# Performance work log

Hardware: AMD Instinct MI355X
Metric: run time of the kernel (lower is better)

The kernel has to match this reference:

```python
import jax, jax.numpy as jnp
import numpy as np

# Irreps structure: (multiplicity, component dim 2l+1) for 64x0e + 32x1o + 16x2e
MULTS = (64, 32, 16)
DIMS = (1, 3, 5)
N_NODES = 65536
NUM_TYPES = 64


def setup_inputs() -> dict:
    key = jax.random.key(0)
    k_x, k_idx, k0, k1, k2 = jax.random.split(key, 5)
    dim = sum(m * d for m, d in zip(MULTS, DIMS))  # 240
    x = jax.random.normal(k_x, (N_NODES, dim), dtype=jnp.float32)
    idx = jax.random.randint(k_idx, (N_NODES,), 0, NUM_TYPES)
    W0 = jax.random.normal(k0, (NUM_TYPES, 64, 64), dtype=jnp.float32)
    W1 = jax.random.normal(k1, (NUM_TYPES, 32, 32), dtype=jnp.float32)
    W2 = jax.random.normal(k2, (NUM_TYPES, 16, 16), dtype=jnp.float32)
    return {"x": x, "W0": W0, "W1": W1, "W2": W2, "idx": idx}


def reference(x, W0, W1, W2, idx):
    """Indexed e3nn-style linear: per-node index gathers a weight set; each
    irrep block mixes multiplicity channels (shared across the 2l+1 components)
    with e3nn path normalization 1/sqrt(m_in)."""
    n = x.shape[0]
    outs = []
    off = 0
    for W, m, d in zip((W0, W1, W2), MULTS, DIMS):
        blk = x[:, off:off + m * d].reshape(n, m, d)  # [N, m_in, 2l+1]
        off += m * d
        Wn = W[idx]  # gather per-node weights: [N, m_in, m_out]
        scale = np.float32(1.0 / np.sqrt(m))
        out = jnp.einsum('nio,nid->nod', Wn, blk) * scale  # [N, m_out, 2l+1]
        outs.append(out.reshape(n, m * d))
    return jnp.concatenate(outs, axis=-1)
```

## Files before the change

kernel.cpp:

```cpp
#include <hip/hip_runtime.h>

typedef __attribute__((ext_vector_type(8))) short short8;
typedef __attribute__((ext_vector_type(4))) float floatx4;
typedef __attribute__((ext_vector_type(4))) unsigned uintx4;

#define NTYPES    64
#define WT_STRIDE 5632
#define WROWS     16
#define CPAD      16
#define RSTRIDE   976

__device__ __forceinline__ unsigned short f2bf(float f) {
    union { float f; unsigned u; } v; v.f = f;
    unsigned u = v.u;
    u += 0x7FFFu + ((u >> 16) & 1u);
    return (unsigned short)(u >> 16);
}

__device__ __forceinline__ unsigned pk2(float lo, float hi) {
    unsigned r;
    asm("v_cvt_pk_bf16_f32 %0, %1, %2" : "=v"(r) : "v"(lo), "v"(hi));
    return r;
}

__global__ __launch_bounds__(256) void wt_kernel(const float* __restrict__ W0,
                                                 const float* __restrict__ W1,
                                                 const float* __restrict__ W2,
                                                 const int* __restrict__ idx,
                                                 unsigned short* __restrict__ wt,
                                                 int* __restrict__ bh, int n) {
    __shared__ float ws0[4096];
    __shared__ float ws1[1024];
    __shared__ float ws2[256];
    __shared__ int hc[NTYPES];
    const int t = blockIdx.x, tid = threadIdx.x;
    if (tid < NTYPES) hc[tid] = 0;
    const float4* s0 = (const float4*)(W0 + (size_t)t * 4096);
#pragma unroll
    for (int j = 0; j < 4; ++j) ((float4*)ws0)[j * 256 + tid] = s0[j * 256 + tid];
    ((float4*)ws1)[tid] = ((const float4*)(W1 + (size_t)t * 1024))[tid];
    if (tid < 64) ((float4*)ws2)[tid] = ((const float4*)(W2 + (size_t)t * 256))[tid];
    __syncthreads();
    const int per = (n + NTYPES - 1) / NTYPES;
    for (int e = tid; e < per; e += 256) {
        int g = t * per + e;
        if (g < n) atomicAdd(&hc[idx[g]], 1);
    }
    unsigned short* dst = wt + (size_t)t * WT_STRIDE;
    for (int e = tid; e < 4096; e += 256) {
        int f = e >> 9, rem = e & 511, rr = rem >> 5, k2 = rem & 31;
        int i = (f & 1) * 32 + k2, o = (f >> 1) * 16 + rr;
        dst[e] = f2bf(ws0[i * 64 + o] * 0.125f);
    }
    for (int e = tid; e < 1024; e += 256) {
        int h = e >> 9, rem = e & 511, rr = rem >> 5, k = rem & 31;
        dst[4096 + e] = f2bf(ws1[k * 32 + h * 16 + rr] * 0.17677669529663687f);
    }
    for (int e = tid; e < 512; e += 256) {
        int rr = e >> 5, k = e & 31;
        dst[5120 + e] = (k < 16) ? f2bf(ws2[k * 16 + rr] * 0.25f) : (unsigned short)0;
    }
    __syncthreads();
    if (tid < NTYPES) bh[t * NTYPES + tid] = hc[tid];
}

__global__ __launch_bounds__(64) void base_kernel(const int* __restrict__ bh,
                                                  int* __restrict__ gcur) {
    const int t = threadIdx.x;
    int v = 0;
#pragma unroll
    for (int b = 0; b < NTYPES; ++b) v += bh[b * NTYPES + t];
    int s = v;
#pragma unroll
    for (int o = 1; o < 64; o <<= 1) {
        int u = __shfl_up(s, o);
        if (t >= o) s += u;
    }
    gcur[t * CPAD] = s - v;
}

__global__ __launch_bounds__(256) void scatter_kernel(const int* __restrict__ idx,
                                                      int* __restrict__ gcur,
                                                      int* __restrict__ psort, int n) {
    __shared__ int c[NTYPES], off[NTYPES], cur[NTYPES];
    const int tid = threadIdx.x, g = blockIdx.x * 256 + tid;
    if (tid < NTYPES) { c[tid] = 0; cur[tid] = 0; }
    __syncthreads();
    int ty = -1;
    if (g < n) { ty = idx[g]; atomicAdd(&c[ty], 1); }
    __syncthreads();
    if (tid < NTYPES && c[tid]) off[tid] = atomicAdd(&gcur[tid * CPAD], c[tid]);
    __syncthreads();
    if (g < n) {
        int rk = atomicAdd(&cur[ty], 1);
        psort[off[ty] + rk] = g | (ty << 24);
    }
}

#define LOAD_FRAGS(WB) do {                                         \
    const unsigned short* _wp = (WB) + r * 32 + q4 * 8;             \
    wa0 = *(const short8*)(_wp);                                    \
    wa1 = *(const short8*)(_wp + 512);                              \
    wa2 = *(const short8*)(_wp + 1024);                             \
    wa3 = *(const short8*)(_wp + 1536);                             \
    wa4 = *(const short8*)(_wp + 2048);                             \
    wa5 = *(const short8*)(_wp + 2560);                             \
    wa6 = *(const short8*)(_wp + 3072);                             \
    wa7 = *(const short8*)(_wp + 3584);                             \
    wc0 = *(const short8*)(_wp + 4096);                             \
    wc1 = *(const short8*)(_wp + 4608);                             \
    wc2 = *(const short8*)(_wp + 5120);                             \
} while (0)

__global__ __launch_bounds__(64) void main_kernel(
    const float* __restrict__ x,
    const int* __restrict__ psort,
    const unsigned short* __restrict__ wt,
    float* __restrict__ out, int n)
{
    __shared__ __align__(16) unsigned char xl[16384];
    const int ln = threadIdx.x;
    const int nbase = blockIdx.x * WROWS;
    if (nbase >= n) return;
    const int nv = min(WROWS, n - nbase);

    int pl = 0;
    if (ln < WROWS && (nbase + ln) < n) pl = psort[nbase + ln];

    const int r = ln & 15, q4 = ln >> 4;

    int ti  = __shfl(pl, r) >> 24;
    int tim = __shfl(pl, (r > 0) ? (r - 1) : 0) >> 24;
    bool bnd = (r == 0) || (ti != tim);
    unsigned m = (unsigned)(__ballot(bnd) & 0xFFFFull);
    const int ty0 = __shfl(pl, 0) >> 24;

#pragma unroll
    for (int k = 0; k < 16; ++k) {
        int L = k * 1024 + ln * 16;
        int row = (int)(((unsigned)(L >> 4) * 1075u) >> 16);
        int col = L - row * RSTRIDE;
        int node = __shfl(pl, min(row, 15)) & 0xFFFFFF;
        int colc = min(col, 944);
        const float* src = x + (size_t)node * 240 + (colc >> 2);
        __builtin_amdgcn_global_load_lds(
            (const __attribute__((address_space(1))) void*)src,
            (__attribute__((address_space(3))) void*)(xl + k * 1024),
            16, 0, 0);
    }

    short8 wa0, wa1, wa2, wa3, wa4, wa5, wa6, wa7, wc0, wc1, wc2;
    LOAD_FRAGS(wt + (size_t)ty0 * WT_STRIDE);

    asm volatile("s_waitcnt vmcnt(0)" ::: "memory");
    __builtin_amdgcn_sched_barrier(0);

    const float4* xr = (const float4*)(xl + r * RSTRIDE);
    float4 f0a = xr[q4 * 2],     f0b = xr[q4 * 2 + 1];
    float4 f0c = xr[8 + q4 * 2], f0d = xr[9 + q4 * 2];
    float4 g0 = xr[16 + q4 * 6],     g1 = xr[16 + q4 * 6 + 1], g2 = xr[16 + q4 * 6 + 2];
    float4 g3 = xr[16 + q4 * 6 + 3], g4 = xr[16 + q4 * 6 + 4], g5 = xr[16 + q4 * 6 + 5];
    const int hb = 40 + (q4 & 1) * 10;
    float4 h0 = xr[hb],     h1 = xr[hb + 1], h2 = xr[hb + 2], h3 = xr[hb + 3];
    float4 h4 = xr[hb + 4], h5 = xr[hb + 5], h6 = xr[hb + 6], h7 = xr[hb + 7];
    float4 h8 = xr[hb + 8], h9 = xr[hb + 9];

    union frag { short8 s; uintx4 u; };

    frag bx0, bx1;
    bx0.u = uintx4{pk2(f0a.x, f0a.y), pk2(f0a.z, f0a.w),
                   pk2(f0b.x, f0b.y), pk2(f0b.z, f0b.w)};
    bx1.u = uintx4{pk2(f0c.x, f0c.y), pk2(f0c.z, f0c.w),
                   pk2(f0d.x, f0d.y), pk2(f0d.z, f0d.w)};
    const float G[24] = {g0.x, g0.y, g0.z, g0.w, g1.x, g1.y, g1.z, g1.w,
                         g2.x, g2.y, g2.z, g2.w, g3.x, g3.y, g3.z, g3.w,
                         g4.x, g4.y, g4.z, g4.w, g5.x, g5.y, g5.z, g5.w};
    frag b1d[3];
#pragma unroll
    for (int d = 0; d < 3; ++d)
        b1d[d].u = uintx4{pk2(G[d], G[3 + d]), pk2(G[6 + d], G[9 + d]),
                          pk2(G[12 + d], G[15 + d]), pk2(G[18 + d], G[21 + d])};
    const float H[40] = {h0.x, h0.y, h0.z, h0.w, h1.x, h1.y, h1.z, h1.w,
                         h2.x, h2.y, h2.z, h2.w, h3.x, h3.y, h3.z, h3.w,
                         h4.x, h4.y, h4.z, h4.w, h5.x, h5.y, h5.z, h5.w,
                         h6.x, h6.y, h6.z, h6.w, h7.x, h7.y, h7.z, h7.w,
                         h8.x, h8.y, h8.z, h8.w, h9.x, h9.y, h9.z, h9.w};
    frag b2d[5];
#pragma unroll
    for (int d = 0; d < 5; ++d)
        b2d[d].u = uintx4{pk2(H[d], H[5 + d]), pk2(H[10 + d], H[15 + d]),
                          pk2(H[20 + d], H[25 + d]), pk2(H[30 + d], H[35 + d])};

    const bool vrow = (r < nv);
    const int node_r = __shfl(pl, min(r, nv - 1)) & 0xFFFFFF;
    float* op = out + (size_t)node_r * 240;

    while (true) {
        const int slo = __builtin_ctz(m);
        const unsigned m2 = m & (m - 1u);
        const int shi = m2 ? __builtin_ctz(m2) : nv;
        const bool vst = vrow && (r >= slo) && (r < shi);

        {
            floatx4 ac;
            ac = floatx4{0.f, 0.f, 0.f, 0.f};
            ac = __builtin_amdgcn_mfma_f32_16x16x32_bf16(wa0, bx0.s, ac, 0, 0, 0);
            ac = __builtin_amdgcn_mfma_f32_16x16x32_bf16(wa1, bx1.s, ac, 0, 0, 0);
            if (vst) *(floatx4*)(op + q4 * 4) = ac;
            ac = floatx4{0.f, 0.f, 0.f, 0.f};
            ac = __builtin_amdgcn_mfma_f32_16x16x32_bf16(wa2, bx0.s, ac, 0, 0, 0);
            ac = __builtin_amdgcn_mfma_f32_16x16x32_bf16(wa3, bx1.s, ac, 0, 0, 0);
            if (vst) *(floatx4*)(op + 16 + q4 * 4) = ac;
            ac = floatx4{0.f, 0.f, 0.f, 0.f};
            ac = __builtin_amdgcn_mfma_f32_16x16x32_bf16(wa4, bx0.s, ac, 0, 0, 0);
            ac = __builtin_amdgcn_mfma_f32_16x16x32_bf16(wa5, bx1.s, ac, 0, 0, 0);
            if (vst) *(floatx4*)(op + 32 + q4 * 4) = ac;
            ac = floatx4{0.f, 0.f, 0.f, 0.f};
            ac = __builtin_amdgcn_mfma_f32_16x16x32_bf16(wa6, bx0.s, ac, 0, 0, 0);
            ac = __builtin_amdgcn_mfma_f32_16x16x32_bf16(wa7, bx1.s, ac, 0, 0, 0);
            if (vst) *(floatx4*)(op + 48 + q4 * 4) = ac;
        }

        {
            floatx4 a1[2][3];
#pragma unroll
            for (int d = 0; d < 3; ++d) {
                floatx4 z = {0.f, 0.f, 0.f, 0.f};
                a1[0][d] = __builtin_amdgcn_mfma_f32_16x16x32_bf16(wc0, b1d[d].s, z, 0, 0, 0);
                a1[1][d] = __builtin_amdgcn_mfma_f32_16x16x32_bf16(wc1, b1d[d].s, z, 0, 0, 0);
            }
            if (vst) {
#pragma unroll
                for (int h = 0; h < 2; ++h) {
                    float* o1 = op + 64 + (h * 16 + q4 * 4) * 3;
                    floatx4 v0 = {a1[h][0][0], a1[h][1][0], a1[h][2][0], a1[h][0][1]};
                    floatx4 v1 = {a1[h][1][1], a1[h][2][1], a1[h][0][2], a1[h][1][2]};
                    floatx4 v2 = {a1[h][2][2], a1[h][0][3], a1[h][1][3], a1[h][2][3]};
                    *(floatx4*)(o1)     = v0;
                    *(floatx4*)(o1 + 4) = v1;
                    *(floatx4*)(o1 + 8) = v2;
                }
            }
        }

        {
            floatx4 a2[5];
#pragma unroll
            for (int d = 0; d < 5; ++d) {
                floatx4 z = {0.f, 0.f, 0.f, 0.f};
                a2[d] = __builtin_amdgcn_mfma_f32_16x16x32_bf16(wc2, b2d[d].s, z, 0, 0, 0);
            }
            if (vst) {
                float* o2 = op + 160 + q4 * 20;
                floatx4 v0 = {a2[0][0], a2[1][0], a2[2][0], a2[3][0]};
                floatx4 v1 = {a2[4][0], a2[0][1], a2[1][1], a2[2][1]};
                floatx4 v2 = {a2[3][1], a2[4][1], a2[0][2], a2[1][2]};
                floatx4 v3 = {a2[2][2], a2[3][2], a2[4][2], a2[0][3]};
                floatx4 v4 = {a2[1][3], a2[2][3], a2[3][3], a2[4][3]};
                *(floatx4*)(o2)      = v0;
                *(floatx4*)(o2 + 4)  = v1;
                *(floatx4*)(o2 + 8)  = v2;
                *(floatx4*)(o2 + 12) = v3;
                *(floatx4*)(o2 + 16) = v4;
            }
        }

        m = m2;
        if (!m) break;
        const int tyn = __shfl(pl, __builtin_ctz(m)) >> 24;
        LOAD_FRAGS(wt + (size_t)tyn * WT_STRIDE);
    }
}

extern "C" void kernel_launch(void* const* d_in, const int* in_sizes, int n_in,
                              void* d_out, int out_size, void* d_ws, size_t ws_size,
                              hipStream_t stream) {
    const float* x  = (const float*)d_in[0];
    const float* W0 = (const float*)d_in[1];
    const float* W1 = (const float*)d_in[2];
    const float* W2 = (const float*)d_in[3];
    const int*   idx = (const int*)d_in[4];
    float* out = (float*)d_out;
    const int n = in_sizes[4];
    const int nb = (n + 255) / 256;

    char* ws = (char*)d_ws;
    unsigned short* wt = (unsigned short*)ws;
    size_t off = (size_t)NTYPES * WT_STRIDE * 2;
    int* psort = (int*)(ws + off); off += (size_t)n * 4;
    int* bh    = (int*)(ws + off); off += (size_t)NTYPES * NTYPES * 4;
    int* gcur  = (int*)(ws + off);

    wt_kernel     <<<NTYPES, 256, 0, stream>>>(W0, W1, W2, idx, wt, bh, n);
    base_kernel   <<<1, 64, 0, stream>>>(bh, gcur);
    scatter_kernel<<<nb, 256, 0, stream>>>(idx, gcur, psort, n);
    main_kernel   <<<(n + WROWS - 1) / WROWS, 64, 0, stream>>>(x, psort, wt, out, n);
}
```

Before: 143.6 us.

## Process four 16-row windows per block with double-buffered LDS prefetch

Each block now handles four consecutive 16-node windows instead of one. Each window's x rows are gathered into LDS asynchronously while the previous window runs its MFMAs, using two LDS buffers and a partial vmcnt wait. Predicated stores are replaced by branch-free stores: rows that should not be written send their store to a scratch sink buffer in the workspace. This aims to hide gather latency and cut per-block launch overhead. The costs are fewer blocks (less parallelism across CUs), twice the LDS per block, extra sink write traffic, and a hand-tuned vmcnt count that must match the number of outstanding loads.

```diff
diff --git a/kernel.cpp b/kernel.cpp
--- a/kernel.cpp
+++ b/kernel.cpp
@@ -7,6 +7,7 @@
 #define NTYPES    64
 #define WT_STRIDE 5632
 #define WROWS     16
+#define NWIN      4
 #define CPAD      16
 #define RSTRIDE   976
 
@@ -112,163 +113,174 @@
     wc2 = *(const short8*)(_wp + 5120);                             \
 } while (0)
 
+#define STAGE(buf, win) do {                                                     \
+    _Pragma("unroll")                                                            \
+    for (int k = 0; k < 16; ++k) {                                               \
+        int L = k * 1024 + ln * 16;                                              \
+        int row = (int)(((unsigned)(L >> 4) * 1075u) >> 16);                     \
+        int col = L - row * RSTRIDE;                                             \
+        int node = __shfl(pe, (win) * 16 + min(row, 15)) & 0xFFFFFF;             \
+        int colc = min(col, 944);                                                \
+        const float* src = x + (size_t)node * 240 + (colc >> 2);                 \
+        __builtin_amdgcn_global_load_lds(                                        \
+            (const __attribute__((address_space(1))) void*)src,                  \
+            (__attribute__((address_space(3))) void*)(xl[buf] + k * 1024),       \
+            16, 0, 0);                                                           \
+    }                                                                            \
+} while (0)
+
 __global__ __launch_bounds__(64) void main_kernel(
     const float* __restrict__ x,
     const int* __restrict__ psort,
     const unsigned short* __restrict__ wt,
-    float* __restrict__ out, int n)
+    float* __restrict__ out, float* __restrict__ sink, int n)
 {
-    __shared__ __align__(16) unsigned char xl[16384];
+    __shared__ __align__(16) unsigned char xl[2][16384];
     const int ln = threadIdx.x;
-    const int nbase = blockIdx.x * WROWS;
-    if (nbase >= n) return;
-    const int nv = min(WROWS, n - nbase);
-
-    int pl = 0;
-    if (ln < WROWS && (nbase + ln) < n) pl = psort[nbase + ln];
-
     const int r = ln & 15, q4 = ln >> 4;
-
-    int ti  = __shfl(pl, r) >> 24;
-    int tim = __shfl(pl, (r > 0) ? (r - 1) : 0) >> 24;
-    bool bnd = (r == 0) || (ti != tim);
-    unsigned m = (unsigned)(__ballot(bnd) & 0xFFFFull);
-    const int ty0 = __shfl(pl, 0) >> 24;
-
-#pragma unroll
-    for (int k = 0; k < 16; ++k) {
-        int L = k * 1024 + ln * 16;
-        int row = (int)(((unsigned)(L >> 4) * 1075u) >> 16);
-        int col = L - row * RSTRIDE;
-        int node = __shfl(pl, min(row, 15)) & 0xFFFFFF;
-        int colc = min(col, 944);
-        const float* src = x + (size_t)node * 240 + (colc >> 2);
-        __builtin_amdgcn_global_load_lds(
-            (const __attribute__((address_space(1))) void*)src,
-            (__attribute__((address_space(3))) void*)(xl + k * 1024),
-            16, 0, 0);
-    }
-
-    short8 wa0, wa1, wa2, wa3, wa4, wa5, wa6, wa7, wc0, wc1, wc2;
-    LOAD_FRAGS(wt + (size_t)ty0 * WT_STRIDE);
-
-    asm volatile("s_waitcnt vmcnt(0)" ::: "memory");
-    __builtin_amdgcn_sched_barrier(0);
-
-    const float4* xr = (const float4*)(xl + r * RSTRIDE);
-    float4 f0a = xr[q4 * 2],     f0b = xr[q4 * 2 + 1];
-    float4 f0c = xr[8 + q4 * 2], f0d = xr[9 + q4 * 2];
-    float4 g0 = xr[16 + q4 * 6],     g1 = xr[16 + q4 * 6 + 1], g2 = xr[16 + q4 * 6 + 2];
-    float4 g3 = xr[16 + q4 * 6 + 3], g4 = xr[16 + q4 * 6 + 4], g5 = xr[16 + q4 * 6 + 5];
-    const int hb = 40 + (q4 & 1) * 10;
-    float4 h0 = xr[hb],     h1 = xr[hb + 1], h2 = xr[hb + 2], h3 = xr[hb + 3];
-    float4 h4 = xr[hb + 4], h5 = xr[hb + 5], h6 = xr[hb + 6], h7 = xr[hb + 7];
-    float4 h8 = xr[hb + 8], h9 = xr[hb + 9];
-
-    union frag { short8 s; uintx4 u; };
-
-    frag bx0, bx1;
-    bx0.u = uintx4{pk2(f0a.x, f0a.y), pk2(f0a.z, f0a.w),
-                   pk2(f0b.x, f0b.y), pk2(f0b.z, f0b.w)};
-    bx1.u = uintx4{pk2(f0c.x, f0c.y), pk2(f0c.z, f0c.w),
-                   pk2(f0d.x, f0d.y), pk2(f0d.z, f0d.w)};
-    const float G[24] = {g0.x, g0.y, g0.z, g0.w, g1.x, g1.y, g1.z, g1.w,
-                         g2.x, g2.y, g2.z, g2.w, g3.x, g3.y, g3.z, g3.w,
-                         g4.x, g4.y, g4.z, g4.w, g5.x, g5.y, g5.z, g5.w};
-    frag b1d[3];
-#pragma unroll
-    for (int d = 0; d < 3; ++d)
-        b1d[d].u = uintx4{pk2(G[d], G[3 + d]), pk2(G[6 + d], G[9 + d]),
-                          pk2(G[12 + d], G[15 + d]), pk2(G[18 + d], G[21 + d])};
-    const float H[40] = {h0.x, h0.y, h0.z, h0.w, h1.x, h1.y, h1.z, h1.w,
-                         h2.x, h2.y, h2.z, h2.w, h3.x, h3.y, h3.z, h3.w,
-                         h4.x, h4.y, h4.z, h4.w, h5.x, h5.y, h5.z, h5.w,
-                         h6.x, h6.y, h6.z, h6.w, h7.x, h7.y, h7.z, h7.w,
-                         h8.x, h8.y, h8.z, h8.w, h9.x, h9.y, h9.z, h9.w};
-    frag b2d[5];
-#pragma unroll
-    for (int d = 0; d < 5; ++d)
-        b2d[d].u = uintx4{pk2(H[d], H[5 + d]), pk2(H[10 + d], H[15 + d]),
-                          pk2(H[20 + d], H[25 + d]), pk2(H[30 + d], H[35 + d])};
-
-    const bool vrow = (r < nv);
-    const int node_r = __shfl(pl, min(r, nv - 1)) & 0xFFFFFF;
-    float* op = out + (size_t)node_r * 240;
-
-    while (true) {
-        const int slo = __builtin_ctz(m);
-        const unsigned m2 = m & (m - 1u);
-        const int shi = m2 ? __builtin_ctz(m2) : nv;
-        const bool vst = vrow && (r >= slo) && (r < shi);
-
-        {
-            floatx4 ac;
-            ac = floatx4{0.f, 0.f, 0.f, 0.f};
-            ac = __builtin_amdgcn_mfma_f32_16x16x32_bf16(wa0, bx0.s, ac, 0, 0, 0);
-            ac = __builtin_amdgcn_mfma_f32_16x16x32_bf16(wa1, bx1.s, ac, 0, 0, 0);
-            if (vst) *(floatx4*)(op + q4 * 4) = ac;
-            ac = floatx4{0.f, 0.f, 0.f, 0.f};
-            ac = __builtin_amdgcn_mfma_f32_16x16x32_bf16(wa2, bx0.s, ac, 0, 0, 0);
-            ac = __builtin_amdgcn_mfma_f32_16x16x32_bf16(wa3, bx1.s, ac, 0, 0, 0);
-            if (vst) *(floatx4*)(op + 16 + q4 * 4) = ac;
-            ac = floatx4{0.f, 0.f, 0.f, 0.f};
-            ac = __builtin_amdgcn_mfma_f32_16x16x32_bf16(wa4, bx0.s, ac, 0, 0, 0);
-            ac = __builtin_amdgcn_mfma_f32_16x16x32_bf16(wa5, bx1.s, ac, 0, 0, 0);
-            if (vst) *(floatx4*)(op + 32 + q4 * 4) = ac;
-            ac = floatx4{0.f, 0.f, 0.f, 0.f};
-            ac = __builtin_amdgcn_mfma_f32_16x16x32_bf16(wa6, bx0.s, ac, 0, 0, 0);
-            ac = __builtin_amdgcn_mfma_f32_16x16x32_bf16(wa7, bx1.s, ac, 0, 0, 0);
-            if (vst) *(floatx4*)(op + 48 + q4 * 4) = ac;
-        }
-
-        {
-            floatx4 a1[2][3];
-#pragma unroll
-            for (int d = 0; d < 3; ++d) {
-                floatx4 z = {0.f, 0.f, 0.f, 0.f};
-                a1[0][d] = __builtin_amdgcn_mfma_f32_16x16x32_bf16(wc0, b1d[d].s, z, 0, 0, 0);
-                a1[1][d] = __builtin_amdgcn_mfma_f32_16x16x32_bf16(wc1, b1d[d].s, z, 0, 0, 0);
+    const int gbase = blockIdx.x * (WROWS * NWIN);
+    if (gbase >= n) return;
+
+    int pe = 0;
+    if (gbase + ln < n) pe = psort[gbase + ln];
+
+    float* snk = sink + ln * 4;
+
+    STAGE(0, 0);
+
+#pragma unroll
+    for (int t = 0; t < NWIN; ++t) {
+        const int wb = gbase + t * WROWS;
+        if (wb >= n) break;
+        const int nv = min(WROWS, n - wb);
+        const int buf = t & 1;
+
+        if (t == 0) asm volatile("s_waitcnt vmcnt(0)" ::: "memory");
+        else        asm volatile("s_waitcnt vmcnt(26)" ::: "memory");
+        __builtin_amdgcn_sched_barrier(0);
+
+        const float4* xr = (const float4*)(xl[buf] + r * RSTRIDE);
+        float4 f0a = xr[q4 * 2],     f0b = xr[q4 * 2 + 1];
+        float4 f0c = xr[8 + q4 * 2], f0d = xr[9 + q4 * 2];
+        float4 g0 = xr[16 + q4 * 6],     g1 = xr[16 + q4 * 6 + 1], g2 = xr[16 + q4 * 6 + 2];
+        float4 g3 = xr[16 + q4 * 6 + 3], g4 = xr[16 + q4 * 6 + 4], g5 = xr[16 + q4 * 6 + 5];
+        const int hb = 40 + (q4 & 1) * 10;
+        float4 h0 = xr[hb],     h1 = xr[hb + 1], h2 = xr[hb + 2], h3 = xr[hb + 3];
+        float4 h4 = xr[hb + 4], h5 = xr[hb + 5], h6 = xr[hb + 6], h7 = xr[hb + 7];
+        float4 h8 = xr[hb + 8], h9 = xr[hb + 9];
+
+        if (t + 1 < NWIN && gbase + (t + 1) * WROWS < n) STAGE(buf ^ 1, t + 1);
+
+        int ti  = __shfl(pe, t * 16 + r) >> 24;
+        int tim = __shfl(pe, t * 16 + ((r > 0) ? (r - 1) : 0)) >> 24;
+        bool bnd = (r == 0) || (ti != tim);
+        unsigned m = (unsigned)(__ballot(bnd) & 0xFFFFull);
+        const int ty0 = __shfl(pe, t * 16) >> 24;
+
+        short8 wa0, wa1, wa2, wa3, wa4, wa5, wa6, wa7, wc0, wc1, wc2;
+        LOAD_FRAGS(wt + (size_t)ty0 * WT_STRIDE);
+
+        union frag { short8 s; uintx4 u; };
+        frag bx0, bx1;
+        bx0.u = uintx4{pk2(f0a.x, f0a.y), pk2(f0a.z, f0a.w),
+                       pk2(f0b.x, f0b.y), pk2(f0b.z, f0b.w)};
+        bx1.u = uintx4{pk2(f0c.x, f0c.y), pk2(f0c.z, f0c.w),
+                       pk2(f0d.x, f0d.y), pk2(f0d.z, f0d.w)};
+        const float G[24] = {g0.x, g0.y, g0.z, g0.w, g1.x, g1.y, g1.z, g1.w,
+                             g2.x, g2.y, g2.z, g2.w, g3.x, g3.y, g3.z, g3.w,
+                             g4.x, g4.y, g4.z, g4.w, g5.x, g5.y, g5.z, g5.w};
+        frag b1d[3];
+#pragma unroll
+        for (int d = 0; d < 3; ++d)
+            b1d[d].u = uintx4{pk2(G[d], G[3 + d]), pk2(G[6 + d], G[9 + d]),
+                              pk2(G[12 + d], G[15 + d]), pk2(G[18 + d], G[21 + d])};
+        const float H[40] = {h0.x, h0.y, h0.z, h0.w, h1.x, h1.y, h1.z, h1.w,
+                             h2.x, h2.y, h2.z, h2.w, h3.x, h3.y, h3.z, h3.w,
+                             h4.x, h4.y, h4.z, h4.w, h5.x, h5.y, h5.z, h5.w,
+                             h6.x, h6.y, h6.z, h6.w, h7.x, h7.y, h7.z, h7.w,
+                             h8.x, h8.y, h8.z, h8.w, h9.x, h9.y, h9.z, h9.w};
+        frag b2d[5];
+#pragma unroll
+        for (int d = 0; d < 5; ++d)
+            b2d[d].u = uintx4{pk2(H[d], H[5 + d]), pk2(H[10 + d], H[15 + d]),
+                              pk2(H[20 + d], H[25 + d]), pk2(H[30 + d], H[35 + d])};
+
+        const bool vrow = (r < nv);
+        const int node_r = __shfl(pe, t * 16 + min(r, nv - 1)) & 0xFFFFFF;
+        float* op = out + (size_t)node_r * 240;
+
+        while (true) {
+            const int slo = __builtin_ctz(m);
+            const unsigned m2 = m & (m - 1u);
+            const int shi = m2 ? __builtin_ctz(m2) : nv;
+            const bool vst = vrow && (r >= slo) && (r < shi);
+#define OST(p) ((floatx4*)(vst ? (float*)(p) : snk))
+
+            {
+                floatx4 ac;
+                ac = floatx4{0.f, 0.f, 0.f, 0.f};
+                ac = __builtin_amdgcn_mfma_f32_16x16x32_bf16(wa0, bx0.s, ac, 0, 0, 0);
+                ac = __builtin_amdgcn_mfma_f32_16x16x32_bf16(wa1, bx1.s, ac, 0, 0, 0);
+                *OST(op + q4 * 4) = ac;
+                ac = floatx4{0.f, 0.f, 0.f, 0.f};
+                ac = __builtin_amdgcn_mfma_f32_16x16x32_bf16(wa2, bx0.s, ac, 0, 0, 0);
+                ac = __builtin_amdgcn_mfma_f32_16x16x32_bf16(wa3, bx1.s, ac, 0, 0, 0);
+                *OST(op + 16 + q4 * 4) = ac;
+                ac = floatx4{0.f, 0.f, 0.f, 0.f};
+                ac = __builtin_amdgcn_mfma_f32_16x16x32_bf16(wa4, bx0.s, ac, 0, 0, 0);
+                ac = __builtin_amdgcn_mfma_f32_16x16x32_bf16(wa5, bx1.s, ac, 0, 0, 0);
+                *OST(op + 32 + q4 * 4) = ac;
+                ac = floatx4{0.f, 0.f, 0.f, 0.f};
+                ac = __builtin_amdgcn_mfma_f32_16x16x32_bf16(wa6, bx0.s, ac, 0, 0, 0);
+                ac = __builtin_amdgcn_mfma_f32_16x16x32_bf16(wa7, bx1.s, ac, 0, 0, 0);
+                *OST(op + 48 + q4 * 4) = ac;
             }
-            if (vst) {
+
+            {
+                floatx4 a1[2][3];
+#pragma unroll
+                for (int d = 0; d < 3; ++d) {
+                    floatx4 z = {0.f, 0.f, 0.f, 0.f};
+                    a1[0][d] = __builtin_amdgcn_mfma_f32_16x16x32_bf16(wc0, b1d[d].s, z, 0, 0, 0);
+                    a1[1][d] = __builtin_amdgcn_mfma_f32_16x16x32_bf16(wc1, b1d[d].s, z, 0, 0, 0);
+                }
 #pragma unroll
                 for (int h = 0; h < 2; ++h) {
                     float* o1 = op + 64 + (h * 16 + q4 * 4) * 3;
                     floatx4 v0 = {a1[h][0][0], a1[h][1][0], a1[h][2][0], a1[h][0][1]};
                     floatx4 v1 = {a1[h][1][1], a1[h][2][1], a1[h][0][2], a1[h][1][2]};
                     floatx4 v2 = {a1[h][2][2], a1[h][0][3], a1[h][1][3], a1[h][2][3]};
-                    *(floatx4*)(o1)     = v0;
-                    *(floatx4*)(o1 + 4) = v1;
-                    *(floatx4*)(o1 + 8) = v2;
+                    *OST(o1)     = v0;
+                    *OST(o1 + 4) = v1;
+                    *OST(o1 + 8) = v2;
                 }
             }
-        }
-
-        {
-            floatx4 a2[5];
-#pragma unroll
-            for (int d = 0; d < 5; ++d) {
-                floatx4 z = {0.f, 0.f, 0.f, 0.f};
-                a2[d] = __builtin_amdgcn_mfma_f32_16x16x32_bf16(wc2, b2d[d].s, z, 0, 0, 0);
-            }
-            if (vst) {
+
+            {
+                floatx4 a2[5];
+#pragma unroll
+                for (int d = 0; d < 5; ++d) {
+                    floatx4 z = {0.f, 0.f, 0.f, 0.f};
+                    a2[d] = __builtin_amdgcn_mfma_f32_16x16x32_bf16(wc2, b2d[d].s, z, 0, 0, 0);
+                }
                 float* o2 = op + 160 + q4 * 20;
                 floatx4 v0 = {a2[0][0], a2[1][0], a2[2][0], a2[3][0]};
                 floatx4 v1 = {a2[4][0], a2[0][1], a2[1][1], a2[2][1]};
                 floatx4 v2 = {a2[3][1], a2[4][1], a2[0][2], a2[1][2]};
                 floatx4 v3 = {a2[2][2], a2[3][2], a2[4][2], a2[0][3]};
                 floatx4 v4 = {a2[1][3], a2[2][3], a2[3][3], a2[4][3]};
-                *(floatx4*)(o2)      = v0;
-                *(floatx4*)(o2 + 4)  = v1;
-                *(floatx4*)(o2 + 8)  = v2;
-                *(floatx4*)(o2 + 12) = v3;
-                *(floatx4*)(o2 + 16) = v4;
+                *OST(o2)      = v0;
+                *OST(o2 + 4)  = v1;
+                *OST(o2 + 8)  = v2;
+                *OST(o2 + 12) = v3;
+                *OST(o2 + 16) = v4;
             }
+#undef OST
+            m = m2;
+            if (!m) break;
+            const int tyn = __shfl(pe, t * 16 + __builtin_ctz(m)) >> 24;
+            LOAD_FRAGS(wt + (size_t)tyn * WT_STRIDE);
         }
-
-        m = m2;
-        if (!m) break;
-        const int tyn = __shfl(pl, __builtin_ctz(m)) >> 24;
-        LOAD_FRAGS(wt + (size_t)tyn * WT_STRIDE);
     }
 }
 
@@ -289,10 +301,12 @@
     size_t off = (size_t)NTYPES * WT_STRIDE * 2;
     int* psort = (int*)(ws + off); off += (size_t)n * 4;
     int* bh    = (int*)(ws + off); off += (size_t)NTYPES * NTYPES * 4;
-    int* gcur  = (int*)(ws + off);
+    int* gcur  = (int*)(ws + off); off += (size_t)NTYPES * CPAD * 4;
+    float* sink = (float*)(ws + off);
 
     wt_kernel     <<<NTYPES, 256, 0, stream>>>(W0, W1, W2, idx, wt, bh, n);
     base_kernel   <<<1, 64, 0, stream>>>(bh, gcur);
     scatter_kernel<<<nb, 256, 0, stream>>>(idx, gcur, psort, n);
-    main_kernel   <<<(n + WROWS - 1) / WROWS, 64, 0, stream>>>(x, psort, wt, out, n);
-}
+    const int rows_pb = WROWS * NWIN;
+    main_kernel   <<<(n + rows_pb - 1) / rows_pb, 64, 0, stream>>>(x, psort, wt, out, sink, n);
+}
```

New measurement: 143.6 us. No clear change (+0.0%).
